# Kernel tuning notes

Measured on AMD Instinct MI355X. Metric: run time of the kernel, lower is better.

Reference implementation:

```python
import jax, jax.numpy as jnp
import numpy as np

CTX, H, ENC, BALL = 256, 128, 128, 2
IN_DIM = 2 + BALL + ENC  # prev_disp(2) + ball(2) + encoding(128)
B, T = 8192, 128


def setup_inputs() -> dict:
    key = jax.random.key(0)
    ks = jax.random.split(key, 16)
    s = lambda fan_in: 1.0 / np.sqrt(fan_in)
    inp = {
        "context": jax.random.normal(ks[0], (B, CTX), jnp.float32),
        "target_encoding": jax.random.normal(ks[1], (B, ENC), jnp.float32),
        "ball_land_xy": jax.random.normal(ks[2], (B, BALL), jnp.float32),
        "max_frames": T,
        # context_to_h / context_to_c
        "Wh": jax.random.uniform(ks[3], (H, CTX), jnp.float32, -s(CTX), s(CTX)),
        "bh": jax.random.uniform(ks[4], (H,), jnp.float32, -s(CTX), s(CTX)),
        "Wc": jax.random.uniform(ks[5], (H, CTX), jnp.float32, -s(CTX), s(CTX)),
        "bc": jax.random.uniform(ks[6], (H,), jnp.float32, -s(CTX), s(CTX)),
        # LSTM (PyTorch gate order: i, f, g, o)
        "W_ih": jax.random.uniform(ks[7], (4 * H, IN_DIM), jnp.float32, -s(H), s(H)),
        "W_hh": jax.random.uniform(ks[8], (4 * H, H), jnp.float32, -s(H), s(H)),
        "b_ih": jax.random.uniform(ks[9], (4 * H,), jnp.float32, -s(H), s(H)),
        "b_hh": jax.random.uniform(ks[10], (4 * H,), jnp.float32, -s(H), s(H)),
        # output head
        "Wo": jax.random.uniform(ks[11], (2, H), jnp.float32, -s(H), s(H)),
        "bo": jax.random.uniform(ks[12], (2,), jnp.float32, -s(H), s(H)),
    }
    return inp


def _decode(context, target_encoding, ball_land_xy, Wh, bh, Wc, bc,
            W_ih, W_hh, b_ih, b_hh, Wo, bo, max_frames):
    h0 = context @ Wh.T + bh                      # (B, H)
    c0 = context @ Wc.T + bc                      # (B, H)
    Bn = context.shape[0]
    # split input weights: first 2 cols act on prev_disp, rest on static [ball, enc]
    W_prev = W_ih[:, :2]                          # (4H, 2)
    W_stat = W_ih[:, 2:]                          # (4H, BALL+ENC)
    static_in = jnp.concatenate([ball_land_xy, target_encoding], axis=-1)
    gate_static = static_in @ W_stat.T + b_ih + b_hh  # (B, 4H), constant per step
    Hn = h0.shape[-1]

    def step(carry, _):
        h, c, prev = carry
        gates = prev @ W_prev.T + h @ W_hh.T + gate_static
        i, f, g, o = jnp.split(gates, 4, axis=-1)
        c = jax.nn.sigmoid(f) * c + jax.nn.sigmoid(i) * jnp.tanh(g)
        h = jax.nn.sigmoid(o) * jnp.tanh(c)
        pred = h @ Wo.T + bo                      # (B, 2)
        prev = jax.lax.stop_gradient(pred)        # matches .detach()
        return (h, c, prev), pred

    prev0 = jnp.zeros((Bn, 2), dtype=context.dtype)
    _, preds = jax.lax.scan(step, (h0, c0, prev0), None, length=max_frames)
    return jnp.transpose(preds, (1, 0, 2))        # (B, T, 2)


def reference(context, target_encoding, ball_land_xy, max_frames,
              Wh, bh, Wc, bc, W_ih, W_hh, b_ih, b_hh, Wo, bo):
    return _decode(context, target_encoding, ball_land_xy, Wh, bh, Wc, bc,
                   W_ih, W_hh, b_ih, b_hh, Wo, bo, max_frames)
```

## Files before the change

### kernel.cpp

```cpp
#include <hip/hip_runtime.h>
#include <hip/hip_bf16.h>


#define HDIM 128
#define CTX_DIM 256
#define T_FRAMES 128
#define BB 16
#define STR 136

typedef __bf16 bf16x8 __attribute__((ext_vector_type(8)));
typedef float  f32x4  __attribute__((ext_vector_type(4)));

union frag_u {
  bf16x8 v;
  unsigned short s[8];
  uint4 u4;
};

#if __has_builtin(__builtin_amdgcn_exp2f)
#define EXP2(x) __builtin_amdgcn_exp2f(x)
#else
#define EXP2(x) __expf((x) * 0.6931471805599453f)
#endif
#define RCP(x) __builtin_amdgcn_rcpf(x)

__device__ __forceinline__ unsigned short f2bf(float x) {
  unsigned u = __builtin_bit_cast(unsigned, x);
  u += 0x7FFFu + ((u >> 16) & 1u);
  return (unsigned short)(u >> 16);
}
__device__ __forceinline__ float bf2f(unsigned short h) {
  unsigned u = ((unsigned)h) << 16;
  return __builtin_bit_cast(float, u);
}
template<int CTRL>
__device__ __forceinline__ float dpp_mov(float x) {
  return __builtin_bit_cast(float,
    __builtin_amdgcn_mov_dpp(__builtin_bit_cast(int, x), CTRL, 0xF, 0xF, true));
}
__device__ __forceinline__ float row_reduce16(float v) {
  v += dpp_mov<0xB1>(v);
  v += dpp_mov<0x4E>(v);
  v += dpp_mov<0x124>(v);
  v += dpp_mov<0x128>(v);
  return v;
}

#define MFMA(a, b, c) __builtin_amdgcn_mfma_f32_16x16x32_bf16((a), (b), (c), 0, 0, 0)

__global__ __launch_bounds__(512, 4) void traj_lstm(
    const float* __restrict__ ctx, const float* __restrict__ enc,
    const float* __restrict__ ball,
    const float* __restrict__ Wh, const float* __restrict__ bh,
    const float* __restrict__ Wc, const float* __restrict__ bc,
    const float* __restrict__ W_ih, const float* __restrict__ W_hh,
    const float* __restrict__ b_ih, const float* __restrict__ b_hh,
    const float* __restrict__ Wo, const float* __restrict__ bo,
    float* __restrict__ outp)
{
  __shared__ __align__(16) __bf16 sh_h[2][BB * STR];
  __shared__ __align__(16) unsigned short sh_sA[BB * 264];
  __shared__ __align__(16) unsigned short sh_sB[BB * 264];
  __shared__ __align__(16) float sh_gs[4 * HDIM * 16];
  __shared__ __align__(16) uint4 sh_wof[4 * 64];
  __shared__ float sh_pw0[8][BB * 2];
  __shared__ float sh_p0[BB * 2];

  const int tid  = threadIdx.x;
  const int w    = tid >> 6;
  const int l    = tid & 63;
  const int q    = l >> 4;
  const int c16  = l & 15;
  const int colH = w * 16 + c16;
  const int rbase = blockIdx.x * BB;

  const float Lc = 1.4426950408889634f;
  const float SG[4] = {Lc, Lc, 2.f * Lc, Lc};
  const float bo0 = bo[0], bo1 = bo[1];
  const float wo0 = Wo[colH], wo1 = Wo[HDIM + colH];

  float wp0[4], wp1[4];
  #pragma unroll
  for (int g = 0; g < 4; ++g) {
    wp0[g] = W_ih[(size_t)(g * HDIM + colH) * 132 + 0];
    wp1[g] = W_ih[(size_t)(g * HDIM + colH) * 132 + 1];
  }

  frag_u Wf[4][4];
  #pragma unroll
  for (int kt = 0; kt < 4; ++kt) {
    const float* w0p = Wo + kt * 32 + q * 8;
    const float* w1p = Wo + HDIM + kt * 32 + q * 8;
    float4 a0 = *(const float4*)w0p, a1 = *(const float4*)(w0p + 4);
    float4 b0 = *(const float4*)w1p, b1 = *(const float4*)(w1p + 4);
    float wo0v[8] = {a0.x, a0.y, a0.z, a0.w, a1.x, a1.y, a1.z, a1.w};
    float wo1v[8] = {b0.x, b0.y, b0.z, b0.w, b1.x, b1.y, b1.z, b1.w};
    #pragma unroll
    for (int g = 0; g < 4; ++g) {
      const float* wr = W_hh + (size_t)(g * HDIM + colH) * HDIM + kt * 32 + q * 8;
      float4 f0 = *(const float4*)wr;
      float4 f1 = *(const float4*)(wr + 4);
      float ff[8] = {f0.x, f0.y, f0.z, f0.w, f1.x, f1.y, f1.z, f1.w};
      #pragma unroll
      for (int j = 0; j < 8; ++j)
        Wf[g][kt].s[j] = f2bf(SG[g] * (ff[j] + wp0[g] * wo0v[j] + wp1[g] * wo1v[j]));
    }
  }

  #pragma unroll
  for (int kt = 0; kt < 4; ++kt) {
    frag_u wf;
    #pragma unroll
    for (int j = 0; j < 8; ++j) {
      float x = (c16 < 2) ? Wo[c16 * HDIM + kt * 32 + q * 8 + j] : 0.f;
      wf.s[j] = f2bf(x);
    }
    if (w == 0) sh_wof[kt * 64 + l] = wf.u4;
  }

  for (int e = tid; e < BB * 256; e += 512) {
    int row = e >> 8, col = e & 255;
    float x = ctx[(size_t)(rbase + row) * CTX_DIM + col];
    unsigned short hb = f2bf(x);
    sh_sA[row * 264 + col] = hb;
    sh_sB[row * 264 + col] = f2bf(x - bf2f(hb));
  }
  __syncthreads();

  float cst[4];
  {
    f32x4 aH = {0.f,0.f,0.f,0.f};
    f32x4 aC = {0.f,0.f,0.f,0.f};
    #pragma unroll
    for (int kt = 0; kt < 8; ++kt) {
      frag_u Ahi, Alo;
      Ahi.u4 = *(const uint4*)&sh_sA[c16 * 264 + kt * 32 + q * 8];
      Alo.u4 = *(const uint4*)&sh_sB[c16 * 264 + kt * 32 + q * 8];
      frag_u bhi, blo;
      {
        const float* wr = Wh + (size_t)colH * CTX_DIM + kt * 32 + q * 8;
        float4 f0 = *(const float4*)wr;
        float4 f1 = *(const float4*)(wr + 4);
        float ff[8] = {f0.x, f0.y, f0.z, f0.w, f1.x, f1.y, f1.z, f1.w};
        #pragma unroll
        for (int j = 0; j < 8; ++j) {
          unsigned short hb = f2bf(ff[j]);
          bhi.s[j] = hb;
          blo.s[j] = f2bf(ff[j] - bf2f(hb));
        }
      }
      aH = MFMA(Ahi.v, bhi.v, aH);
      aH = MFMA(Alo.v, bhi.v, aH);
      aH = MFMA(Ahi.v, blo.v, aH);
      {
        const float* wr = Wc + (size_t)colH * CTX_DIM + kt * 32 + q * 8;
        float4 f0 = *(const float4*)wr;
        float4 f1 = *(const float4*)(wr + 4);
        float ff[8] = {f0.x, f0.y, f0.z, f0.w, f1.x, f1.y, f1.z, f1.w};
        #pragma unroll
        for (int j = 0; j < 8; ++j) {
          unsigned short hb = f2bf(ff[j]);
          bhi.s[j] = hb;
          blo.s[j] = f2bf(ff[j] - bf2f(hb));
        }
      }
      aC = MFMA(Ahi.v, bhi.v, aC);
      aC = MFMA(Alo.v, bhi.v, aC);
      aC = MFMA(Ahi.v, blo.v, aC);
    }
    float bhv = bh[colH], bcv = bc[colH];
    float pp0[4][2];
    #pragma unroll
    for (int r = 0; r < 4; ++r) {
      float h0v = aH[r] + bhv;
      cst[r] = aC[r] + bcv;
      sh_h[0][(q * 4 + r) * STR + colH] = (__bf16)h0v;
      pp0[r][0] = h0v * wo0;
      pp0[r][1] = h0v * wo1;
    }
    #pragma unroll
    for (int m = 0; m < 4; ++m) {
      pp0[m][0] = row_reduce16(pp0[m][0]);
      pp0[m][1] = row_reduce16(pp0[m][1]);
    }
    if (c16 == 0) {
      #pragma unroll
      for (int r = 0; r < 4; ++r) {
        sh_pw0[w][(q * 4 + r) * 2 + 0] = pp0[r][0];
        sh_pw0[w][(q * 4 + r) * 2 + 1] = pp0[r][1];
      }
    }
  }
  __syncthreads();

  for (int e = tid; e < BB * 168; e += 512) {
    int row = e / 168, col = e - row * 168;
    float x = (col < 2) ? ball[(size_t)(rbase + row) * 2 + col]
            : (col < 130) ? enc[(size_t)(rbase + row) * 128 + (col - 2)] : 0.f;
    unsigned short hb = f2bf(x);
    sh_sA[row * 168 + col] = hb;
    sh_sB[row * 168 + col] = f2bf(x - bf2f(hb));
  }
  if (tid < BB * 2) {
    float s = (tid & 1) ? bo1 : bo0;
    #pragma unroll
    for (int w2 = 0; w2 < 8; ++w2) s += sh_pw0[w2][tid];
    sh_p0[tid] = s;
  }
  __syncthreads();

  {
    f32x4 gacc[4] = {{0.f,0.f,0.f,0.f},{0.f,0.f,0.f,0.f},
                     {0.f,0.f,0.f,0.f},{0.f,0.f,0.f,0.f}};
    #pragma unroll
    for (int kt = 0; kt < 5; ++kt) {
      frag_u Ahi, Alo;
      Ahi.u4 = *(const uint4*)&sh_sA[c16 * 168 + kt * 32 + q * 8];
      Alo.u4 = *(const uint4*)&sh_sB[c16 * 168 + kt * 32 + q * 8];
      #pragma unroll
      for (int g = 0; g < 4; ++g) {
        frag_u bhi, blo;
        #pragma unroll
        for (int j = 0; j < 8; ++j) {
          int kk = kt * 32 + q * 8 + j;
          float x = (kk < 130) ? SG[g] * W_ih[(size_t)(g * HDIM + colH) * 132 + 2 + kk] : 0.f;
          unsigned short hb = f2bf(x);
          bhi.s[j] = hb;
          blo.s[j] = f2bf(x - bf2f(hb));
        }
        gacc[g] = MFMA(Ahi.v, bhi.v, gacc[g]);
        gacc[g] = MFMA(Alo.v, bhi.v, gacc[g]);
        gacc[g] = MFMA(Ahi.v, blo.v, gacc[g]);
      }
    }
    #pragma unroll
    for (int g = 0; g < 4; ++g) {
      int colG = g * HDIM + colH;
      float bb = SG[g] * (b_ih[colG] + b_hh[colG] + bo0 * wp0[g] + bo1 * wp1[g]);
      f32x4 t = gacc[g];
      t[0] += bb; t[1] += bb; t[2] += bb; t[3] += bb;
      *(f32x4*)&sh_gs[((g * HDIM + colH) * 4 + q) * 4] = t;
    }
  }
  float wps0[4], wps1[4];
  #pragma unroll
  for (int g = 0; g < 4; ++g) {
    wps0[g] = SG[g] * wp0[g];
    wps1[g] = SG[g] * wp1[g];
  }

  auto body = [&](int t, int rbuf, bool first) {
    const int wbuf = rbuf ^ 1;
    const __bf16* hp = &sh_h[rbuf][c16 * STR];

    f32x4 acc[4];
    #pragma unroll
    for (int g = 0; g < 4; ++g)
      acc[g] = *(const f32x4*)&sh_gs[((g * HDIM + colH) * 4 + q) * 4];
    f32x4 accP = {0.f, 0.f, 0.f, 0.f};

    #pragma unroll
    for (int kt = 0; kt < 4; ++kt) {
      frag_u A;
      A.u4 = *(const uint4*)(hp + kt * 32 + q * 8);
      #pragma unroll
      for (int g = 0; g < 4; ++g)
        acc[g] = MFMA(A.v, Wf[g][kt].v, acc[g]);
      if (!first && w == 7) {
        frag_u wof;
        wof.u4 = sh_wof[kt * 64 + l];
        accP = MFMA(A.v, wof.v, accP);
      }
    }
    if (first) {
      #pragma unroll
      for (int r = 0; r < 4; ++r) {
        float2 p0r = *(const float2*)&sh_p0[(q * 4 + r) * 2];
        #pragma unroll
        for (int g = 0; g < 4; ++g)
          acc[g][r] -= p0r.x * wps0[g] + p0r.y * wps1[g];
      }
    }
    if (!first && w == 7 && c16 < 2) {
      const int m0 = q * 4;
      const float bov = c16 ? bo1 : bo0;
      #pragma unroll
      for (int r = 0; r < 4; ++r)
        outp[(size_t)(rbase + m0 + r) * (T_FRAMES * 2) + (t - 1) * 2 + c16] = accP[r] + bov;
    }

    __bf16* hw = &sh_h[wbuf][colH];
    #pragma unroll
    for (int r = 0; r < 4; ++r) {
      float ei = EXP2(-acc[0][r]);
      float ef = EXP2(-acc[1][r]);
      float eg = EXP2(-acc[2][r]);
      float eo = EXP2(-acc[3][r]);
      float t1 = (1.f + ei) * (1.f + eg);
      float pf = 1.f + ef;
      float num = cst[r] * t1 + (1.f - eg) * pf;
      float cv = num * RCP(t1 * pf);
      cst[r] = cv;
      float cc = fmaxf(cv, -15.f);
      float ec = EXP2(cc * (-2.f * 1.4426950408889634f));
      float hv = (1.f - ec) * RCP((1.f + eo) * (1.f + ec));
      hw[(q * 4 + r) * STR] = (__bf16)hv;
    }
    __syncthreads();
  };

  body(0, 0, true);
  for (int tp = 0; tp < 63; ++tp) {
    body(2 * tp + 1, 1, false);
    body(2 * tp + 2, 0, false);
  }
  body(127, 1, false);

  if (w == 7) {
    const __bf16* hp = &sh_h[0][c16 * STR];
    f32x4 accP = {0.f, 0.f, 0.f, 0.f};
    #pragma unroll
    for (int kt = 0; kt < 4; ++kt) {
      frag_u A, wof;
      A.u4 = *(const uint4*)(hp + kt * 32 + q * 8);
      wof.u4 = sh_wof[kt * 64 + l];
      accP = MFMA(A.v, wof.v, accP);
    }
    if (c16 < 2) {
      const int m0 = q * 4;
      const float bov = c16 ? bo1 : bo0;
      #pragma unroll
      for (int r = 0; r < 4; ++r)
        outp[(size_t)(rbase + m0 + r) * (T_FRAMES * 2) + 127 * 2 + c16] = accP[r] + bov;
    }
  }
}

extern "C" void kernel_launch(void* const* d_in, const int* in_sizes, int n_in,
                              void* d_out, int out_size, void* d_ws, size_t ws_size,
                              hipStream_t stream) {
  (void)in_sizes; (void)n_in; (void)d_ws; (void)ws_size; (void)out_size;
  const float* ctx  = (const float*)d_in[0];
  const float* enc  = (const float*)d_in[1];
  const float* ball = (const float*)d_in[2];
  const float* Wh   = (const float*)d_in[4];
  const float* bh   = (const float*)d_in[5];
  const float* Wc   = (const float*)d_in[6];
  const float* bc   = (const float*)d_in[7];
  const float* W_ih = (const float*)d_in[8];
  const float* W_hh = (const float*)d_in[9];
  const float* b_ih = (const float*)d_in[10];
  const float* b_hh = (const float*)d_in[11];
  const float* Wo   = (const float*)d_in[12];
  const float* bo   = (const float*)d_in[13];
  float* outp = (float*)d_out;

  dim3 grid(512), block(512);
  traj_lstm<<<grid, block, 0, stream>>>(ctx, enc, ball, Wh, bh, Wc, bc,
                                        W_ih, W_hh, b_ih, b_hh, Wo, bo, outp);
}
```

Before: 358.4 us.

## Alias staging LDS into arena, defer W_hh fragment build, restructure LSTM step body

```diff
diff --git a/kernel.cpp b/kernel.cpp
--- a/kernel.cpp
+++ b/kernel.cpp
@@ -10,6 +10,7 @@
 
 typedef __bf16 bf16x8 __attribute__((ext_vector_type(8)));
 typedef float  f32x4  __attribute__((ext_vector_type(4)));
+typedef float  f32x2  __attribute__((ext_vector_type(2)));
 
 union frag_u {
   bf16x8 v;
@@ -45,6 +46,8 @@
   v += dpp_mov<0x128>(v);
   return v;
 }
+
+template<int N> struct Int { static constexpr int value = N; };
 
 #define MFMA(a, b, c) __builtin_amdgcn_mfma_f32_16x16x32_bf16((a), (b), (c), 0, 0, 0)
 
@@ -59,12 +62,14 @@
     float* __restrict__ outp)
 {
   __shared__ __align__(16) __bf16 sh_h[2][BB * STR];
-  __shared__ __align__(16) unsigned short sh_sA[BB * 264];
-  __shared__ __align__(16) unsigned short sh_sB[BB * 264];
-  __shared__ __align__(16) float sh_gs[4 * HDIM * 16];
+  __shared__ __align__(16) char sh_arena[32768];
   __shared__ __align__(16) uint4 sh_wof[4 * 64];
   __shared__ float sh_pw0[8][BB * 2];
   __shared__ float sh_p0[BB * 2];
+
+  unsigned short* sh_sA = (unsigned short*)sh_arena;
+  unsigned short* sh_sB = sh_sA + BB * 264;
+  f32x4* gseed = (f32x4*)sh_arena;
 
   const int tid  = threadIdx.x;
   const int w    = tid >> 6;
@@ -78,34 +83,6 @@
   const float SG[4] = {Lc, Lc, 2.f * Lc, Lc};
   const float bo0 = bo[0], bo1 = bo[1];
   const float wo0 = Wo[colH], wo1 = Wo[HDIM + colH];
-
-  float wp0[4], wp1[4];
-  #pragma unroll
-  for (int g = 0; g < 4; ++g) {
-    wp0[g] = W_ih[(size_t)(g * HDIM + colH) * 132 + 0];
-    wp1[g] = W_ih[(size_t)(g * HDIM + colH) * 132 + 1];
-  }
-
-  frag_u Wf[4][4];
-  #pragma unroll
-  for (int kt = 0; kt < 4; ++kt) {
-    const float* w0p = Wo + kt * 32 + q * 8;
-    const float* w1p = Wo + HDIM + kt * 32 + q * 8;
-    float4 a0 = *(const float4*)w0p, a1 = *(const float4*)(w0p + 4);
-    float4 b0 = *(const float4*)w1p, b1 = *(const float4*)(w1p + 4);
-    float wo0v[8] = {a0.x, a0.y, a0.z, a0.w, a1.x, a1.y, a1.z, a1.w};
-    float wo1v[8] = {b0.x, b0.y, b0.z, b0.w, b1.x, b1.y, b1.z, b1.w};
-    #pragma unroll
-    for (int g = 0; g < 4; ++g) {
-      const float* wr = W_hh + (size_t)(g * HDIM + colH) * HDIM + kt * 32 + q * 8;
-      float4 f0 = *(const float4*)wr;
-      float4 f1 = *(const float4*)(wr + 4);
-      float ff[8] = {f0.x, f0.y, f0.z, f0.w, f1.x, f1.y, f1.z, f1.w};
-      #pragma unroll
-      for (int j = 0; j < 8; ++j)
-        Wf[g][kt].s[j] = f2bf(SG[g] * (ff[j] + wp0[g] * wo0v[j] + wp1[g] * wo1v[j]));
-    }
-  }
 
   #pragma unroll
   for (int kt = 0; kt < 4; ++kt) {
@@ -209,112 +186,153 @@
   }
   __syncthreads();
 
-  {
-    f32x4 gacc[4] = {{0.f,0.f,0.f,0.f},{0.f,0.f,0.f,0.f},
-                     {0.f,0.f,0.f,0.f},{0.f,0.f,0.f,0.f}};
-    #pragma unroll
-    for (int kt = 0; kt < 5; ++kt) {
-      frag_u Ahi, Alo;
-      Ahi.u4 = *(const uint4*)&sh_sA[c16 * 168 + kt * 32 + q * 8];
-      Alo.u4 = *(const uint4*)&sh_sB[c16 * 168 + kt * 32 + q * 8];
-      #pragma unroll
-      for (int g = 0; g < 4; ++g) {
-        frag_u bhi, blo;
-        #pragma unroll
-        for (int j = 0; j < 8; ++j) {
-          int kk = kt * 32 + q * 8 + j;
-          float x = (kk < 130) ? SG[g] * W_ih[(size_t)(g * HDIM + colH) * 132 + 2 + kk] : 0.f;
-          unsigned short hb = f2bf(x);
-          bhi.s[j] = hb;
-          blo.s[j] = f2bf(x - bf2f(hb));
-        }
-        gacc[g] = MFMA(Ahi.v, bhi.v, gacc[g]);
-        gacc[g] = MFMA(Alo.v, bhi.v, gacc[g]);
-        gacc[g] = MFMA(Ahi.v, blo.v, gacc[g]);
-      }
-    }
+  f32x4 gacc[4] = {{0.f,0.f,0.f,0.f},{0.f,0.f,0.f,0.f},
+                   {0.f,0.f,0.f,0.f},{0.f,0.f,0.f,0.f}};
+  #pragma unroll
+  for (int kt = 0; kt < 5; ++kt) {
+    frag_u Ahi, Alo;
+    Ahi.u4 = *(const uint4*)&sh_sA[c16 * 168 + kt * 32 + q * 8];
+    Alo.u4 = *(const uint4*)&sh_sB[c16 * 168 + kt * 32 + q * 8];
     #pragma unroll
     for (int g = 0; g < 4; ++g) {
-      int colG = g * HDIM + colH;
-      float bb = SG[g] * (b_ih[colG] + b_hh[colG] + bo0 * wp0[g] + bo1 * wp1[g]);
-      f32x4 t = gacc[g];
-      t[0] += bb; t[1] += bb; t[2] += bb; t[3] += bb;
-      *(f32x4*)&sh_gs[((g * HDIM + colH) * 4 + q) * 4] = t;
-    }
-  }
-  float wps0[4], wps1[4];
+      frag_u bhi, blo;
+      #pragma unroll
+      for (int j = 0; j < 8; ++j) {
+        int kk = kt * 32 + q * 8 + j;
+        float x = (kk < 130) ? SG[g] * W_ih[(size_t)(g * HDIM + colH) * 132 + 2 + kk] : 0.f;
+        unsigned short hb = f2bf(x);
+        bhi.s[j] = hb;
+        blo.s[j] = f2bf(x - bf2f(hb));
+      }
+      gacc[g] = MFMA(Ahi.v, bhi.v, gacc[g]);
+      gacc[g] = MFMA(Alo.v, bhi.v, gacc[g]);
+      gacc[g] = MFMA(Ahi.v, blo.v, gacc[g]);
+    }
+  }
+  __syncthreads();
+
+  float wp0[4], wp1[4], wps0[4], wps1[4];
   #pragma unroll
   for (int g = 0; g < 4; ++g) {
+    wp0[g] = W_ih[(size_t)(g * HDIM + colH) * 132 + 0];
+    wp1[g] = W_ih[(size_t)(g * HDIM + colH) * 132 + 1];
     wps0[g] = SG[g] * wp0[g];
     wps1[g] = SG[g] * wp1[g];
-  }
-
-  auto body = [&](int t, int rbuf, bool first) {
-    const int wbuf = rbuf ^ 1;
-    const __bf16* hp = &sh_h[rbuf][c16 * STR];
+    int colG = g * HDIM + colH;
+    float bb = SG[g] * (b_ih[colG] + b_hh[colG] + bo0 * wp0[g] + bo1 * wp1[g]);
+    f32x4 s = gacc[g];
+    #pragma unroll
+    for (int r = 0; r < 4; ++r) {
+      float2 p0r = *(const float2*)&sh_p0[(q * 4 + r) * 2];
+      s[r] += bb - (p0r.x * wps0[g] + p0r.y * wps1[g]);
+    }
+    gseed[g * 512 + tid] = s;
+  }
+
+  frag_u Wf[4][4];
+  #pragma unroll
+  for (int kt = 0; kt < 4; ++kt) {
+    const float* w0p = Wo + kt * 32 + q * 8;
+    const float* w1p = Wo + HDIM + kt * 32 + q * 8;
+    float4 a0 = *(const float4*)w0p, a1 = *(const float4*)(w0p + 4);
+    float4 b0 = *(const float4*)w1p, b1 = *(const float4*)(w1p + 4);
+    float wo0v[8] = {a0.x, a0.y, a0.z, a0.w, a1.x, a1.y, a1.z, a1.w};
+    float wo1v[8] = {b0.x, b0.y, b0.z, b0.w, b1.x, b1.y, b1.z, b1.w};
+    #pragma unroll
+    for (int g = 0; g < 4; ++g) {
+      const float* wr = W_hh + (size_t)(g * HDIM + colH) * HDIM + kt * 32 + q * 8;
+      float4 f0 = *(const float4*)wr;
+      float4 f1 = *(const float4*)(wr + 4);
+      float ff[8] = {f0.x, f0.y, f0.z, f0.w, f1.x, f1.y, f1.z, f1.w};
+      #pragma unroll
+      for (int j = 0; j < 8; ++j)
+        Wf[g][kt].s[j] = f2bf(SG[g] * (ff[j] + wp0[g] * wo0v[j] + wp1[g] * wo1v[j]));
+    }
+  }
+
+  auto body = [&](auto RC, int t, bool doPred) {
+    constexpr int RBUF = decltype(RC)::value;
+    constexpr int WB = RBUF ^ 1;
+    const __bf16* hp = &sh_h[RBUF][c16 * STR];
+
+    frag_u A[4];
+    #pragma unroll
+    for (int kt = 0; kt < 4; ++kt)
+      A[kt].u4 = *(const uint4*)(hp + kt * 32 + q * 8);
 
     f32x4 acc[4];
+    __builtin_amdgcn_s_setprio(1);
     #pragma unroll
     for (int g = 0; g < 4; ++g)
-      acc[g] = *(const f32x4*)&sh_gs[((g * HDIM + colH) * 4 + q) * 4];
-    f32x4 accP = {0.f, 0.f, 0.f, 0.f};
-
-    #pragma unroll
-    for (int kt = 0; kt < 4; ++kt) {
-      frag_u A;
-      A.u4 = *(const uint4*)(hp + kt * 32 + q * 8);
+      acc[g] = MFMA(A[0].v, Wf[g][0].v, gseed[g * 512 + tid]);
+    #pragma unroll
+    for (int kt = 1; kt < 4; ++kt)
       #pragma unroll
       for (int g = 0; g < 4; ++g)
-        acc[g] = MFMA(A.v, Wf[g][kt].v, acc[g]);
-      if (!first && w == 7) {
+        acc[g] = MFMA(A[kt].v, Wf[g][kt].v, acc[g]);
+
+    if (doPred && w == 7) {
+      f32x4 accP = {0.f, 0.f, 0.f, 0.f};
+      #pragma unroll
+      for (int kt = 0; kt < 4; ++kt) {
         frag_u wof;
         wof.u4 = sh_wof[kt * 64 + l];
-        accP = MFMA(A.v, wof.v, accP);
-      }
-    }
-    if (first) {
-      #pragma unroll
-      for (int r = 0; r < 4; ++r) {
-        float2 p0r = *(const float2*)&sh_p0[(q * 4 + r) * 2];
+        accP = MFMA(A[kt].v, wof.v, accP);
+      }
+      if (c16 < 2) {
+        const float bov = c16 ? bo1 : bo0;
         #pragma unroll
-        for (int g = 0; g < 4; ++g)
-          acc[g][r] -= p0r.x * wps0[g] + p0r.y * wps1[g];
-      }
-    }
-    if (!first && w == 7 && c16 < 2) {
-      const int m0 = q * 4;
-      const float bov = c16 ? bo1 : bo0;
-      #pragma unroll
-      for (int r = 0; r < 4; ++r)
-        outp[(size_t)(rbase + m0 + r) * (T_FRAMES * 2) + (t - 1) * 2 + c16] = accP[r] + bov;
-    }
-
-    __bf16* hw = &sh_h[wbuf][colH];
-    #pragma unroll
-    for (int r = 0; r < 4; ++r) {
-      float ei = EXP2(-acc[0][r]);
-      float ef = EXP2(-acc[1][r]);
-      float eg = EXP2(-acc[2][r]);
-      float eo = EXP2(-acc[3][r]);
-      float t1 = (1.f + ei) * (1.f + eg);
-      float pf = 1.f + ef;
-      float num = cst[r] * t1 + (1.f - eg) * pf;
-      float cv = num * RCP(t1 * pf);
-      cst[r] = cv;
-      float cc = fmaxf(cv, -15.f);
-      float ec = EXP2(cc * (-2.f * 1.4426950408889634f));
-      float hv = (1.f - ec) * RCP((1.f + eo) * (1.f + ec));
-      hw[(q * 4 + r) * STR] = (__bf16)hv;
+        for (int r = 0; r < 4; ++r)
+          outp[(size_t)(rbase + q * 4 + r) * (T_FRAMES * 2) + (t - 1) * 2 + c16] = accP[r] + bov;
+      }
+    }
+    __builtin_amdgcn_s_setprio(0);
+
+    __bf16* hwp = &sh_h[WB][colH];
+    #pragma unroll
+    for (int pr = 0; pr < 2; ++pr) {
+      const int r0 = pr * 2, r1 = pr * 2 + 1;
+      f32x2 ei = { EXP2(-acc[0][r0]), EXP2(-acc[0][r1]) };
+      f32x2 ef = { EXP2(-acc[1][r0]), EXP2(-acc[1][r1]) };
+      f32x2 eg = { EXP2(-acc[2][r0]), EXP2(-acc[2][r1]) };
+      f32x2 eo = { EXP2(-acc[3][r0]), EXP2(-acc[3][r1]) };
+      f32x2 t1 = (1.f + ei) * (1.f + eg);
+      f32x2 pf = 1.f + ef;
+      f32x2 cp = { cst[r0], cst[r1] };
+      f32x2 num = cp * t1 + (1.f - eg) * pf;
+      f32x2 den = t1 * pf;
+      f32x2 cv = num * (f32x2){ RCP(den.x), RCP(den.y) };
+      cst[r0] = cv.x;
+      cst[r1] = cv.y;
+      f32x2 cc = { fmaxf(cv.x, -15.f), fmaxf(cv.y, -15.f) };
+      cc = cc * (-2.f * 1.4426950408889634f);
+      f32x2 ec = { EXP2(cc.x), EXP2(cc.y) };
+      f32x2 d2 = (1.f + eo) * (1.f + ec);
+      f32x2 hv = (1.f - ec) * (f32x2){ RCP(d2.x), RCP(d2.y) };
+      hwp[(q * 4 + r0) * STR] = (__bf16)hv.x;
+      hwp[(q * 4 + r1) * STR] = (__bf16)hv.y;
     }
     __syncthreads();
   };
 
-  body(0, 0, true);
+  body(Int<0>{}, 0, false);
+
+  #pragma unroll
+  for (int g = 0; g < 4; ++g) {
+    f32x4 s = gseed[g * 512 + tid];
+    #pragma unroll
+    for (int r = 0; r < 4; ++r) {
+      float2 p0r = *(const float2*)&sh_p0[(q * 4 + r) * 2];
+      s[r] += p0r.x * wps0[g] + p0r.y * wps1[g];
+    }
+    gseed[g * 512 + tid] = s;
+  }
+
   for (int tp = 0; tp < 63; ++tp) {
-    body(2 * tp + 1, 1, false);
-    body(2 * tp + 2, 0, false);
-  }
-  body(127, 1, false);
+    body(Int<1>{}, 2 * tp + 1, true);
+    body(Int<0>{}, 2 * tp + 2, true);
+  }
+  body(Int<1>{}, 127, true);
 
   if (w == 7) {
     const __bf16* hp = &sh_h[0][c16 * STR];
@@ -327,11 +345,10 @@
       accP = MFMA(A.v, wof.v, accP);
     }
     if (c16 < 2) {
-      const int m0 = q * 4;
       const float bov = c16 ? bo1 : bo0;
       #pragma unroll
       for (int r = 0; r < 4; ++r)
-        outp[(size_t)(rbase + m0 + r) * (T_FRAMES * 2) + 127 * 2 + c16] = accP[r] + bov;
+        outp[(size_t)(rbase + q * 4 + r) * (T_FRAMES * 2) + 127 * 2 + c16] = accP[r] + bov;
     }
   }
 }
```

After: 289.3 us. -19.3%, faster.
